# Performance work log

Measured on AMD Instinct MI355X. Metric: run time of the kernel, lower is better.

Reference implementation:

```python
import jax, jax.numpy as jnp
import numpy as np

D_MODEL = 1024
N_HEADS = 16
D_K = D_MODEL // N_HEADS
D_FF = 4096
EPS = 1e-5


def setup_inputs() -> dict:
    key = jax.random.key(0)
    ks = jax.random.split(key, 16)
    s = 0.02
    d, f = D_MODEL, D_FF
    return {
        'ebd_x': jax.random.normal(ks[0], (2, 2048, d), jnp.float32),
        'Wq': jax.random.normal(ks[1], (d, d), jnp.float32) * s,
        'bq': jnp.zeros((d,), jnp.float32),
        'Wk': jax.random.normal(ks[2], (d, d), jnp.float32) * s,
        'bk': jnp.zeros((d,), jnp.float32),
        'Wv': jax.random.normal(ks[3], (d, d), jnp.float32) * s,
        'bv': jnp.zeros((d,), jnp.float32),
        'Wo': jax.random.normal(ks[4], (d, d), jnp.float32) * s,
        'bo': jnp.zeros((d,), jnp.float32),
        'W1': jax.random.normal(ks[5], (d, f), jnp.float32) * s,
        'b1': jnp.zeros((f,), jnp.float32),
        'W2': jax.random.normal(ks[6], (f, d), jnp.float32) * s,
        'b2': jnp.zeros((d,), jnp.float32),
        'g1': jnp.ones((d,), jnp.float32),
        'beta1': jnp.zeros((d,), jnp.float32),
        'g2': jnp.ones((d,), jnp.float32),
        'beta2': jnp.zeros((d,), jnp.float32),
    }


def _layernorm(x, g, b):
    mu = jnp.mean(x, axis=-1, keepdims=True)
    var = jnp.mean(jnp.square(x - mu), axis=-1, keepdims=True)
    return (x - mu) * jax.lax.rsqrt(var + EPS) * g + b


def reference(ebd_x, Wq, bq, Wk, bk, Wv, bv, Wo, bo, W1, b1, W2, b2, g1, beta1, g2, beta2):
    b, L, d = ebd_x.shape
    h, dk = N_HEADS, D_K
    # QKV projections, split heads: (b, h, L, dk)
    q = (ebd_x @ Wq + bq).reshape(b, L, h, dk).transpose(0, 2, 1, 3)
    k = (ebd_x @ Wk + bk).reshape(b, L, h, dk).transpose(0, 2, 1, 3)
    v = (ebd_x @ Wv + bv).reshape(b, L, h, dk).transpose(0, 2, 1, 3)
    scores = jnp.einsum('bhLd,bhld->bhLl', q, k) / jnp.sqrt(jnp.float32(dk))
    attn = jax.nn.softmax(scores, axis=-1)
    attn_v = jnp.einsum('bhLl,bhld->bhLd', attn, v)
    # faithful to source: reshape (b,h,L,dk) -> (b,L,d) WITHOUT transposing back
    attn_v = attn_v.reshape(b, L, d)
    attn_v = attn_v @ Wo + bo
    # dropout is identity in eval mode
    x1 = _layernorm(attn_v + ebd_x, g1, beta1)
    ff = jax.nn.gelu(x1 @ W1 + b1, approximate=False) @ W2 + b2
    return _layernorm(ff + x1, g2, beta2)
```

## Files before the change

kernel.cpp:

```cpp
#include <hip/hip_runtime.h>
#include <hip/hip_bf16.h>
#include <math.h>

typedef __bf16 bhalf;
typedef __bf16 bhalf8 __attribute__((ext_vector_type(8)));
typedef float  floatx4 __attribute__((ext_vector_type(4)));
typedef float  floatx8 __attribute__((ext_vector_type(8)));
typedef unsigned short ushort_t;
typedef unsigned short ushort8 __attribute__((ext_vector_type(8)));

#define MFMA16(a, b, c) __builtin_amdgcn_mfma_f32_16x16x32_bf16((a), (b), (c), 0, 0, 0)

__device__ __forceinline__ void gload_lds16(const bhalf* g, bhalf* l)
{
    __builtin_amdgcn_global_load_lds((const __attribute__((address_space(1))) void*)g,
                                     (__attribute__((address_space(3))) void*)l, 16, 0, 0);
}

enum { EPI_PLAIN = 0, EPI_RES = 1, EPI_GELU = 2, EPI_QKV = 3 };

__global__ __launch_bounds__(256) void detect_dtype(const ushort_t* __restrict__ x,
                                                    int* __restrict__ flag)
{
    __shared__ int tot;
    if (threadIdx.x == 0) tot = 0;
    __syncthreads();
    int cnt = 0;
#pragma unroll
    for (int it = 0; it < 8; ++it) {
        const ushort8 u = *(const ushort8*)(x + ((size_t)(it * 256 + threadIdx.x)) * 8);
#pragma unroll
        for (int j = 0; j < 8; j += 2) {
            const int e = (u[j] >> 7) & 0xFF;
            if (e >= 0x90) ++cnt;
        }
    }
    atomicAdd(&tot, cnt);
    __syncthreads();
    if (threadIdx.x == 0) flag[0] = (tot > 64) ? 1 : 0;
}

__global__ __launch_bounds__(256) void norm_x(const void* __restrict__ s,
                                              bhalf* __restrict__ d,
                                              const int* __restrict__ flag)
{
    const int i = (blockIdx.x * 256 + threadIdx.x) * 8;
    if (*flag) {
        const floatx8 v = *(const floatx8*)((const float*)s + i);
        bhalf8 o;
#pragma unroll
        for (int j = 0; j < 8; ++j) o[j] = (bhalf)v[j];
        *(bhalf8*)(d + i) = o;
    } else {
        *(ushort8*)((ushort_t*)d + i) = *(const ushort8*)((const ushort_t*)s + i);
    }
}

struct Cvt { const void* s; bhalf* d; int n; };
struct CvtArr { Cvt t[10]; };

__global__ __launch_bounds__(256) void norm_vec(CvtArr a, const int* __restrict__ flag)
{
    const Cvt c = a.t[blockIdx.y];
    const int i = (blockIdx.x * 256 + threadIdx.x) * 8;
    if (i >= c.n) return;
    if (*flag) {
        const floatx8 v = *(const floatx8*)((const float*)c.s + i);
        bhalf8 o;
#pragma unroll
        for (int j = 0; j < 8; ++j) o[j] = (bhalf)v[j];
        *(bhalf8*)(c.d + i) = o;
    } else {
        *(ushort8*)((ushort_t*)c.d + i) = *(const ushort8*)((const ushort_t*)c.s + i);
    }
}

struct TDesc { const void* src; bhalf* dst; int R, C; };
struct TDescArr { TDesc t[6]; };

__global__ __launch_bounds__(256) void transpose_all(TDescArr a, const int* __restrict__ flag)
{
    __shared__ bhalf sm[32][33];
    const int id = blockIdx.x;
    TDesc d;
    int rem;
    if (id < 4096)      { d = a.t[id >> 10]; rem = id & 1023; }
    else if (id < 8192) { d = a.t[4];        rem = id - 4096; }
    else                { d = a.t[5];        rem = id - 8192; }
    const int txc = d.C >> 5;
    const int bx = (rem % txc) * 32;
    const int by = (rem / txc) * 32;
    const int tx = threadIdx.x & 31;
    const int ty = threadIdx.x >> 5;
    if (*flag) {
        const float* fin = (const float*)d.src;
#pragma unroll
        for (int i = 0; i < 4; ++i)
            sm[ty + i * 8][tx] = (bhalf)fin[(size_t)(by + ty + i * 8) * d.C + bx + tx];
    } else {
        const bhalf* bin = (const bhalf*)d.src;
#pragma unroll
        for (int i = 0; i < 4; ++i)
            sm[ty + i * 8][tx] = bin[(size_t)(by + ty + i * 8) * d.C + bx + tx];
    }
    __syncthreads();
#pragma unroll
    for (int i = 0; i < 4; ++i)
        d.dst[(size_t)(bx + ty + i * 8) * d.R + by + tx] = sm[tx][ty + i * 8];
}

__global__ __launch_bounds__(256) void vt_transpose(const bhalf* __restrict__ Vw,
                                                    bhalf* __restrict__ Vt)
{
    __shared__ bhalf sm[32][33];
    const int bh = blockIdx.z;
    const int b = bh >> 4, h = bh & 15;
    const int tb = blockIdx.y * 32;
    const int db = blockIdx.x * 32;
    const int tx = threadIdx.x & 31;
    const int ty = threadIdx.x >> 5;
#pragma unroll
    for (int i = 0; i < 4; ++i)
        sm[ty + i * 8][tx] = Vw[(size_t)(b * 2048 + tb + ty + i * 8) * 1024 + h * 64 + db + tx];
    __syncthreads();
#pragma unroll
    for (int i = 0; i < 4; ++i)
        Vt[(size_t)(bh * 64 + db + ty + i * 8) * 2048 + tb + tx] = sm[tx][ty + i * 8];
}

template <int EPI>
__global__ __launch_bounds__(256) void gemm128(
    const bhalf* __restrict__ A, int lda,
    const bhalf* __restrict__ BT, int ldb,
    const bhalf* __restrict__ bias,
    const bhalf* __restrict__ resid,
    bhalf* __restrict__ C, int ldc, int K, int nbx,
    bhalf* __restrict__ Ck, bhalf* __restrict__ Cv)
{
    __shared__ __align__(16) bhalf As[2][128 * 64];
    __shared__ __align__(16) bhalf Bs[2][64 * 64];

    const int tid  = threadIdx.x;
    const int lane = tid & 63;
    const int w    = tid >> 6;
    const int l15  = lane & 15;
    const int q    = lane >> 4;
    const int wm   = w * 32;

    const int nwg = gridDim.x;
    const int cpx = nwg >> 3;
    const int id  = (blockIdx.x & 7) * cpx + (blockIdx.x >> 3);
    const int n0  = (id % nbx) * 64;
    const int m0  = (id / nbx) * 128;

    const int r8 = lane >> 3;
    const int c8 = lane & 7;
    const int gc = (c8 ^ r8) << 3;

    floatx4 acc[2][4];
#pragma unroll
    for (int i = 0; i < 2; ++i)
#pragma unroll
        for (int j = 0; j < 4; ++j) acc[i][j] = (floatx4){0.f, 0.f, 0.f, 0.f};

    auto stage = [&](int buf, int k0) {
#pragma unroll
        for (int i = 0; i < 4; ++i) {
            const int rb = w * 32 + i * 8;
            gload_lds16(A + (size_t)(m0 + rb + r8) * lda + k0 + gc, &As[buf][rb * 64] + lane * 8);
        }
#pragma unroll
        for (int i = 0; i < 2; ++i) {
            const int rb = w * 16 + i * 8;
            gload_lds16(BT + (size_t)(n0 + rb + r8) * ldb + k0 + gc, &Bs[buf][rb * 64] + lane * 8);
        }
    };

    stage(0, 0);
    const int NT = K >> 6;
    for (int t = 0; t < NT; ++t) {
        const int cur = t & 1;
        __syncthreads();
        if (t + 1 < NT) stage(cur ^ 1, (t + 1) << 6);

#pragma unroll
        for (int s = 0; s < 2; ++s) {
            const int pc = (((s * 4 + q) ^ (l15 & 7)) << 3);
            bhalf8 af[2], bf[4];
#pragma unroll
            for (int mt = 0; mt < 2; ++mt)
                af[mt] = *(const bhalf8*)&As[cur][(wm + mt * 16 + l15) * 64 + pc];
#pragma unroll
            for (int nt = 0; nt < 4; ++nt)
                bf[nt] = *(const bhalf8*)&Bs[cur][(nt * 16 + l15) * 64 + pc];
#pragma unroll
            for (int mt = 0; mt < 2; ++mt)
#pragma unroll
                for (int nt = 0; nt < 4; ++nt)
                    acc[mt][nt] = MFMA16(af[mt], bf[nt], acc[mt][nt]);
        }
    }

#pragma unroll
    for (int mt = 0; mt < 2; ++mt)
#pragma unroll
        for (int nt = 0; nt < 4; ++nt) {
            const int col = n0 + nt * 16 + l15;
            const float bv = (float)bias[col];
#pragma unroll
            for (int r = 0; r < 4; ++r) {
                const int row = m0 + wm + mt * 16 + q * 4 + r;
                float v = acc[mt][nt][r] + bv;
                if constexpr (EPI == EPI_RES) {
                    v += (float)resid[(size_t)row * ldc + col];
                    C[(size_t)row * ldc + col] = (bhalf)v;
                } else if constexpr (EPI == EPI_GELU) {
                    v = 0.5f * v * (1.f + erff(v * 0.70710678118654752f));
                    C[(size_t)row * ldc + col] = (bhalf)v;
                } else if constexpr (EPI == EPI_QKV) {
                    if (col < 1024)       C [(size_t)row * 1024 + col]        = (bhalf)v;
                    else if (col < 2048)  Ck[(size_t)row * 1024 + col - 1024] = (bhalf)v;
                    else                  Cv[(size_t)row * 1024 + col - 2048] = (bhalf)v;
                } else {
                    C[(size_t)row * ldc + col] = (bhalf)v;
                }
            }
        }
}

__global__ __launch_bounds__(256) void flash_attn(
    const bhalf* __restrict__ Q, const bhalf* __restrict__ Km,
    const bhalf* __restrict__ Vt, bhalf* __restrict__ ctx)
{
    __shared__ __align__(16) bhalf Ks[2][64 * 64];
    __shared__ __align__(16) bhalf Vs[2][64 * 64];

    const int tid  = threadIdx.x;
    const int lane = tid & 63;
    const int wq   = tid >> 6;
    const int l15  = lane & 15;
    const int q    = lane >> 4;
    const int bh   = blockIdx.x & 31;
    const int l0   = (blockIdx.x >> 5) * 64;
    const int b    = bh >> 4, h = bh & 15;
    const float SC = 0.125f * 1.44269504f;

    const bhalf* qp = Q + ((size_t)(b * 2048 + l0 + wq * 16 + l15)) * 1024 + h * 64 + q * 8;
    const bhalf8 aQ0 = *(const bhalf8*)qp;
    const bhalf8 aQ1 = *(const bhalf8*)(qp + 32);

    float ps = 0.f;
    floatx4 o[4];
#pragma unroll
    for (int ot = 0; ot < 4; ++ot) o[ot] = (floatx4){0.f, 0.f, 0.f, 0.f};

    const int r8 = lane >> 3;
    const int c8 = lane & 7;
    const bhalf* kbase = Km + ((size_t)(b * 2048)) * 1024 + h * 64;
    const bhalf* vbase = Vt + ((size_t)(bh * 64)) * 2048;

    auto stage = [&](int buf, int kt) {
#pragma unroll
        for (int i = 0; i < 2; ++i) {
            const int rb = wq * 16 + i * 8;
            const int fk = (((rb >> 3) << 1) ^ r8) & 7;
            gload_lds16(kbase + (size_t)(kt + rb + r8) * 1024 + ((c8 ^ fk) << 3),
                        &Ks[buf][rb * 64] + lane * 8);
            gload_lds16(vbase + (size_t)(rb + r8) * 2048 + kt + ((c8 ^ r8) << 3),
                        &Vs[buf][rb * 64] + lane * 8);
        }
    };

    stage(0, 0);
    int cur = 0;
    for (int kt = 0; kt < 2048; kt += 64) {
        __syncthreads();
        if (kt + 64 < 2048) stage(cur ^ 1, kt + 64);

        floatx4 s[4];
#pragma unroll
        for (int nt = 0; nt < 4; ++nt) {
            const int row = (nt >> 1) * 32 + (nt & 1) * 4 + ((l15 >> 2) << 3) + (l15 & 3);
            const int f = (((row >> 3) << 1) ^ row) & 7;
            const bhalf8 k0 = *(const bhalf8*)&Ks[cur][row * 64 + ((q ^ f) << 3)];
            const bhalf8 k1 = *(const bhalf8*)&Ks[cur][row * 64 + (((4 + q) ^ f) << 3)];
            floatx4 z = (floatx4){0.f, 0.f, 0.f, 0.f};
            z = MFMA16(k0, aQ0, z);
            s[nt] = MFMA16(k1, aQ1, z);
        }

        bhalf8 pa[2];
#pragma unroll
        for (int nt = 0; nt < 4; ++nt)
#pragma unroll
            for (int r = 0; r < 4; ++r) {
                const float pv = __builtin_amdgcn_exp2f(fmaf(s[nt][r], SC, -8.f));
                ps += pv;
                pa[nt >> 1][(nt & 1) * 4 + r] = (bhalf)pv;
            }

#pragma unroll
        for (int kc = 0; kc < 2; ++kc)
#pragma unroll
            for (int ot = 0; ot < 4; ++ot) {
                const bhalf8 bV = *(const bhalf8*)&Vs[cur][(ot * 16 + l15) * 64 + (((kc * 4 + q) ^ (l15 & 7)) << 3)];
                o[ot] = MFMA16(pa[kc], bV, o[ot]);
            }
        cur ^= 1;
    }

    ps += __shfl_xor(ps, 16);
    ps += __shfl_xor(ps, 32);
    const float invq = 1.f / ps;
    float inv[4];
#pragma unroll
    for (int r = 0; r < 4; ++r)
        inv[r] = __shfl(invq, (lane & 48) | (q * 4 + r));

#pragma unroll
    for (int ot = 0; ot < 4; ++ot)
#pragma unroll
        for (int r = 0; r < 4; ++r) {
            const int l = l0 + wq * 16 + q * 4 + r;
            const int kk = ot * 16 + l15;
            const int R = h * 128 + (l >> 4);
            const int Cc = (l & 15) * 64 + kk;
            ctx[((size_t)(b * 2048 + R)) * 1024 + Cc] = (bhalf)(o[ot][r] * inv[r]);
        }
}

__global__ __launch_bounds__(256) void ln_kernel(
    const bhalf* __restrict__ X, const bhalf* __restrict__ g,
    const bhalf* __restrict__ be, void* __restrict__ out, const int* __restrict__ flag)
{
    __shared__ float red[4][2];
    const int tid = threadIdx.x;
    const int wid = tid >> 6;
    const int rid = tid >> 7;
    const int lt  = tid & 127;
    const int row = blockIdx.x * 2 + rid;
    const int col = lt * 8;
    const bhalf8 xv = *(const bhalf8*)(X + (size_t)row * 1024 + col);
    float v[8], s1 = 0.f, s2 = 0.f;
#pragma unroll
    for (int i = 0; i < 8; ++i) {
        v[i] = (float)xv[i];
        s1 += v[i];
        s2 += v[i] * v[i];
    }
#pragma unroll
    for (int off = 1; off < 64; off <<= 1) {
        s1 += __shfl_xor(s1, off);
        s2 += __shfl_xor(s2, off);
    }
    if ((tid & 63) == 0) { red[wid][0] = s1; red[wid][1] = s2; }
    __syncthreads();
    const float t1 = red[rid * 2][0] + red[rid * 2 + 1][0];
    const float t2 = red[rid * 2][1] + red[rid * 2 + 1][1];
    const float mu = t1 * (1.f / 1024.f);
    const float rs = rsqrtf(t2 * (1.f / 1024.f) - mu * mu + 1e-5f);
    const bool f32 = flag && (*flag != 0);
    if (f32) {
        floatx8 ov;
#pragma unroll
        for (int i = 0; i < 8; ++i)
            ov[i] = ((v[i] - mu) * rs) * (float)g[col + i] + (float)be[col + i];
        *(floatx8*)((float*)out + (size_t)row * 1024 + col) = ov;
    } else {
        bhalf8 ov;
#pragma unroll
        for (int i = 0; i < 8; ++i)
            ov[i] = (bhalf)(((v[i] - mu) * rs) * (float)g[col + i] + (float)be[col + i]);
        *(bhalf8*)((bhalf*)out + (size_t)row * 1024 + col) = ov;
    }
}

extern "C" void kernel_launch(void* const* d_in, const int* in_sizes, int n_in,
                              void* d_out, int out_size, void* d_ws, size_t ws_size,
                              hipStream_t stream)
{
    (void)in_sizes; (void)n_in; (void)out_size; (void)ws_size;

    char* p = (char*)d_ws;
    const size_t MB = 1024 * 1024;
    int*   flag  = (int*)p;
    bhalf* vecs  = (bhalf*)(p + 128 * 1024);
    bhalf* Qw    = (bhalf*)(p + 1 * MB);
    bhalf* Kw    = (bhalf*)(p + 9 * MB);
    bhalf* Vw    = (bhalf*)(p + 17 * MB);
    bhalf* Vt    = (bhalf*)(p + 25 * MB);
    bhalf* x_n   = (bhalf*)(p + 33 * MB);
    bhalf* WqkvT = (bhalf*)(p + 41 * MB);
    bhalf* WoT   = (bhalf*)(p + 47 * MB);
    bhalf* W1T   = (bhalf*)(p + 49 * MB);
    bhalf* W2T   = (bhalf*)(p + 57 * MB);
    bhalf* ctx   = Vw;
    bhalf* ff1   = (bhalf*)(p + 17 * MB);
    bhalf* ln1   = Qw;
    bhalf* x1    = Kw;
    bhalf* ff2   = Qw;

    bhalf* bqkv  = vecs;
    bhalf* bo_n  = vecs + 1 * 4096;
    bhalf* b1_n  = vecs + 2 * 4096;
    bhalf* b2_n  = vecs + 3 * 4096;
    bhalf* g1_n  = vecs + 4 * 4096;
    bhalf* be1_n = vecs + 5 * 4096;
    bhalf* g2_n  = vecs + 6 * 4096;
    bhalf* be2_n = vecs + 7 * 4096;

    const dim3 blk(256);

    detect_dtype<<<1, blk, 0, stream>>>((const ushort_t*)d_in[0], flag);

    norm_x<<<2048, blk, 0, stream>>>(d_in[0], x_n, flag);
    CvtArr arr;
    arr.t[0] = {d_in[2],  bqkv,        1024};
    arr.t[1] = {d_in[4],  bqkv + 1024, 1024};
    arr.t[2] = {d_in[6],  bqkv + 2048, 1024};
    arr.t[3] = {d_in[8],  bo_n,        1024};
    arr.t[4] = {d_in[10], b1_n,        4096};
    arr.t[5] = {d_in[12], b2_n,        1024};
    arr.t[6] = {d_in[13], g1_n,        1024};
    arr.t[7] = {d_in[14], be1_n,       1024};
    arr.t[8] = {d_in[15], g2_n,        1024};
    arr.t[9] = {d_in[16], be2_n,       1024};
    norm_vec<<<dim3(2, 10), blk, 0, stream>>>(arr, flag);

    TDescArr td;
    td.t[0] = {d_in[1],  WqkvT,               1024, 1024};
    td.t[1] = {d_in[3],  WqkvT + 1024 * 1024, 1024, 1024};
    td.t[2] = {d_in[5],  WqkvT + 2048 * 1024, 1024, 1024};
    td.t[3] = {d_in[7],  WoT,                 1024, 1024};
    td.t[4] = {d_in[9],  W1T,                 1024, 4096};
    td.t[5] = {d_in[11], W2T,                 4096, 1024};
    transpose_all<<<12288, blk, 0, stream>>>(td, flag);

    gemm128<EPI_QKV><<<1536, blk, 0, stream>>>(
        x_n, 1024, WqkvT, 1024, bqkv, nullptr, Qw, 1024, 1024, 48, Kw, Vw);

    vt_transpose<<<dim3(2, 64, 32), blk, 0, stream>>>(Vw, Vt);

    flash_attn<<<1024, blk, 0, stream>>>(Qw, Kw, Vt, ctx);

    gemm128<EPI_RES><<<512, blk, 0, stream>>>(
        ctx, 1024, WoT, 1024, bo_n, x_n, ln1, 1024, 1024, 16, nullptr, nullptr);
    ln_kernel<<<2048, blk, 0, stream>>>(ln1, g1_n, be1_n, x1, nullptr);

    gemm128<EPI_GELU><<<2048, blk, 0, stream>>>(
        x1, 1024, W1T, 1024, b1_n, nullptr, ff1, 4096, 1024, 64, nullptr, nullptr);
    gemm128<EPI_RES><<<512, blk, 0, stream>>>(
        ff1, 4096, W2T, 4096, b2_n, x1, ff2, 1024, 4096, 16, nullptr, nullptr);
    ln_kernel<<<2048, blk, 0, stream>>>(ff2, g2_n, be2_n, d_out, flag);
}
```

Baseline: 380.2 us.

## Rewrite GEMM with 128x128 tiles, 512 threads and triple-buffered LDS pipeline

```diff
diff --git a/kernel.cpp b/kernel.cpp
--- a/kernel.cpp
+++ b/kernel.cpp
@@ -129,7 +129,7 @@
 }
 
 template <int EPI>
-__global__ __launch_bounds__(256) void gemm128(
+__global__ __launch_bounds__(512, 2) void gemm_pp(
     const bhalf* __restrict__ A, int lda,
     const bhalf* __restrict__ BT, int ldb,
     const bhalf* __restrict__ bias,
@@ -137,75 +137,102 @@
     bhalf* __restrict__ C, int ldc, int K, int nbx,
     bhalf* __restrict__ Ck, bhalf* __restrict__ Cv)
 {
-    __shared__ __align__(16) bhalf As[2][128 * 64];
-    __shared__ __align__(16) bhalf Bs[2][64 * 64];
+    extern __shared__ __align__(16) bhalf sm[];
 
     const int tid  = threadIdx.x;
     const int lane = tid & 63;
     const int w    = tid >> 6;
     const int l15  = lane & 15;
     const int q    = lane >> 4;
-    const int wm   = w * 32;
+    const int wm   = (w >> 2) * 64;
+    const int wn   = (w & 3) * 32;
 
     const int nwg = gridDim.x;
     const int cpx = nwg >> 3;
     const int id  = (blockIdx.x & 7) * cpx + (blockIdx.x >> 3);
-    const int n0  = (id % nbx) * 64;
+    const int n0  = (id % nbx) * 128;
     const int m0  = (id / nbx) * 128;
 
-    const int r8 = lane >> 3;
-    const int c8 = lane & 7;
-    const int gc = (c8 ^ r8) << 3;
-
-    floatx4 acc[2][4];
-#pragma unroll
-    for (int i = 0; i < 2; ++i)
-#pragma unroll
-        for (int j = 0; j < 4; ++j) acc[i][j] = (floatx4){0.f, 0.f, 0.f, 0.f};
+    const int r6  = tid >> 3;
+    const int c8t = tid & 7;
+    const bhalf* gA[2]; const bhalf* gB[2]; int lA[2], lB[2];
+#pragma unroll
+    for (int i = 0; i < 2; ++i) {
+        const int row = i * 64 + r6;
+        const int gc  = (c8t ^ (r6 & 7)) << 3;
+        gA[i] = A  + (size_t)(m0 + row) * lda + gc;
+        gB[i] = BT + (size_t)(n0 + row) * ldb + gc;
+        lA[i] = row * 64 + c8t * 8;
+        lB[i] = row * 64 + c8t * 8;
+    }
+
+    floatx4 acc[4][2];
+#pragma unroll
+    for (int i = 0; i < 4; ++i)
+#pragma unroll
+        for (int j = 0; j < 2; ++j) acc[i][j] = (floatx4){0.f, 0.f, 0.f, 0.f};
 
     auto stage = [&](int buf, int k0) {
-#pragma unroll
-        for (int i = 0; i < 4; ++i) {
-            const int rb = w * 32 + i * 8;
-            gload_lds16(A + (size_t)(m0 + rb + r8) * lda + k0 + gc, &As[buf][rb * 64] + lane * 8);
-        }
-#pragma unroll
-        for (int i = 0; i < 2; ++i) {
-            const int rb = w * 16 + i * 8;
-            gload_lds16(BT + (size_t)(n0 + rb + r8) * ldb + k0 + gc, &Bs[buf][rb * 64] + lane * 8);
-        }
+        bhalf* as = sm + buf * 8192;
+        bhalf* bs = sm + 24576 + buf * 8192;
+        gload_lds16(gA[0] + k0, as + lA[0]);
+        gload_lds16(gA[1] + k0, as + lA[1]);
+        gload_lds16(gB[0] + k0, bs + lB[0]);
+        gload_lds16(gB[1] + k0, bs + lB[1]);
     };
 
     stage(0, 0);
+    stage(1, 64);
+    asm volatile("s_waitcnt vmcnt(4)" ::: "memory");
+    __builtin_amdgcn_s_barrier();
+    asm volatile("" ::: "memory");
+
     const int NT = K >> 6;
     for (int t = 0; t < NT; ++t) {
-        const int cur = t & 1;
-        __syncthreads();
-        if (t + 1 < NT) stage(cur ^ 1, (t + 1) << 6);
-
-#pragma unroll
-        for (int s = 0; s < 2; ++s) {
-            const int pc = (((s * 4 + q) ^ (l15 & 7)) << 3);
-            bhalf8 af[2], bf[4];
-#pragma unroll
-            for (int mt = 0; mt < 2; ++mt)
-                af[mt] = *(const bhalf8*)&As[cur][(wm + mt * 16 + l15) * 64 + pc];
-#pragma unroll
-            for (int nt = 0; nt < 4; ++nt)
-                bf[nt] = *(const bhalf8*)&Bs[cur][(nt * 16 + l15) * 64 + pc];
-#pragma unroll
-            for (int mt = 0; mt < 2; ++mt)
-#pragma unroll
-                for (int nt = 0; nt < 4; ++nt)
-                    acc[mt][nt] = MFMA16(af[mt], bf[nt], acc[mt][nt]);
-        }
-    }
-
-#pragma unroll
-    for (int mt = 0; mt < 2; ++mt)
-#pragma unroll
-        for (int nt = 0; nt < 4; ++nt) {
-            const int col = n0 + nt * 16 + l15;
+        const int buf = t % 3;
+        const bhalf* as = sm + buf * 8192;
+        const bhalf* bs = sm + 24576 + buf * 8192;
+
+        bhalf8 af[2][4], bf[2][2];
+#pragma unroll
+        for (int ks = 0; ks < 2; ++ks) {
+            const int pc = (((ks * 4 + q) ^ (l15 & 7)) << 3);
+#pragma unroll
+            for (int mt = 0; mt < 4; ++mt)
+                af[ks][mt] = *(const bhalf8*)&as[(wm + mt * 16 + l15) * 64 + pc];
+#pragma unroll
+            for (int nt = 0; nt < 2; ++nt)
+                bf[ks][nt] = *(const bhalf8*)&bs[(wn + nt * 16 + l15) * 64 + pc];
+        }
+
+        if (t + 2 < NT) stage((t + 2) % 3, (t + 2) << 6);
+
+        __builtin_amdgcn_s_setprio(1);
+#pragma unroll
+        for (int ks = 0; ks < 2; ++ks)
+#pragma unroll
+            for (int mt = 0; mt < 4; ++mt)
+#pragma unroll
+                for (int nt = 0; nt < 2; ++nt)
+                    acc[mt][nt] = MFMA16(af[ks][mt], bf[ks][nt], acc[mt][nt]);
+        __builtin_amdgcn_s_setprio(0);
+
+        if (t + 2 < NT) {
+            asm volatile("s_waitcnt vmcnt(4)" ::: "memory");
+        } else if (t + 1 < NT) {
+            asm volatile("s_waitcnt vmcnt(0)" ::: "memory");
+        }
+        if (t + 1 < NT) {
+            __builtin_amdgcn_s_barrier();
+            asm volatile("" ::: "memory");
+        }
+    }
+
+#pragma unroll
+    for (int mt = 0; mt < 4; ++mt)
+#pragma unroll
+        for (int nt = 0; nt < 2; ++nt) {
+            const int col = n0 + wn + nt * 16 + l15;
             const float bv = (float)bias[col];
 #pragma unroll
             for (int r = 0; r < 4; ++r) {
@@ -409,7 +436,19 @@
     bhalf* g2_n  = vecs + 6 * 4096;
     bhalf* be2_n = vecs + 7 * 4096;
 
+    static bool attr_done = false;
+    if (!attr_done) {
+        hipFuncSetAttribute((const void*)gemm_pp<EPI_QKV>,
+                            hipFuncAttributeMaxDynamicSharedMemorySize, 98304);
+        hipFuncSetAttribute((const void*)gemm_pp<EPI_GELU>,
+                            hipFuncAttributeMaxDynamicSharedMemorySize, 98304);
+        hipFuncSetAttribute((const void*)gemm_pp<EPI_RES>,
+                            hipFuncAttributeMaxDynamicSharedMemorySize, 98304);
+        attr_done = true;
+    }
+
     const dim3 blk(256);
+    const dim3 blk512(512);
 
     detect_dtype<<<1, blk, 0, stream>>>((const ushort_t*)d_in[0], flag);
 
@@ -436,20 +475,20 @@
     td.t[5] = {d_in[11], W2T,                 4096, 1024};
     transpose_all<<<12288, blk, 0, stream>>>(td, flag);
 
-    gemm128<EPI_QKV><<<1536, blk, 0, stream>>>(
-        x_n, 1024, WqkvT, 1024, bqkv, nullptr, Qw, 1024, 1024, 48, Kw, Vw);
+    gemm_pp<EPI_QKV><<<768, blk512, 98304, stream>>>(
+        x_n, 1024, WqkvT, 1024, bqkv, nullptr, Qw, 1024, 1024, 24, Kw, Vw);
 
     vt_transpose<<<dim3(2, 64, 32), blk, 0, stream>>>(Vw, Vt);
 
     flash_attn<<<1024, blk, 0, stream>>>(Qw, Kw, Vt, ctx);
 
-    gemm128<EPI_RES><<<512, blk, 0, stream>>>(
-        ctx, 1024, WoT, 1024, bo_n, x_n, ln1, 1024, 1024, 16, nullptr, nullptr);
+    gemm_pp<EPI_RES><<<256, blk512, 98304, stream>>>(
+        ctx, 1024, WoT, 1024, bo_n, x_n, ln1, 1024, 1024, 8, nullptr, nullptr);
     ln_kernel<<<2048, blk, 0, stream>>>(ln1, g1_n, be1_n, x1, nullptr);
 
-    gemm128<EPI_GELU><<<2048, blk, 0, stream>>>(
-        x1, 1024, W1T, 1024, b1_n, nullptr, ff1, 4096, 1024, 64, nullptr, nullptr);
-    gemm128<EPI_RES><<<512, blk, 0, stream>>>(
-        ff1, 4096, W2T, 4096, b2_n, x1, ff2, 1024, 4096, 16, nullptr, nullptr);
+    gemm_pp<EPI_GELU><<<1024, blk512, 98304, stream>>>(
+        x1, 1024, W1T, 1024, b1_n, nullptr, ff1, 4096, 1024, 32, nullptr, nullptr);
+    gemm_pp<EPI_RES><<<256, blk512, 98304, stream>>>(
+        ff1, 4096, W2T, 4096, b2_n, x1, ff2, 1024, 4096, 8, nullptr, nullptr);
     ln_kernel<<<2048, blk, 0, stream>>>(ff2, g2_n, be2_n, d_out, flag);
 }
```

New measurement: 360.7 us. 1.05x faster.

## Triple-buffer GEMM LDS staging with prefetch distance two and single barrier

Applied to the files above, without the earlier changes.

```diff
diff --git a/kernel.cpp b/kernel.cpp
--- a/kernel.cpp
+++ b/kernel.cpp
@@ -129,7 +129,7 @@
 }
 
 template <int EPI>
-__global__ __launch_bounds__(256) void gemm128(
+__global__ __launch_bounds__(256) void gemm_3b(
     const bhalf* __restrict__ A, int lda,
     const bhalf* __restrict__ BT, int ldb,
     const bhalf* __restrict__ bias,
@@ -137,8 +137,7 @@
     bhalf* __restrict__ C, int ldc, int K, int nbx,
     bhalf* __restrict__ Ck, bhalf* __restrict__ Cv)
 {
-    __shared__ __align__(16) bhalf As[2][128 * 64];
-    __shared__ __align__(16) bhalf Bs[2][64 * 64];
+    extern __shared__ __align__(16) bhalf sm[];
 
     const int tid  = threadIdx.x;
     const int lane = tid & 63;
@@ -163,41 +162,68 @@
 #pragma unroll
         for (int j = 0; j < 4; ++j) acc[i][j] = (floatx4){0.f, 0.f, 0.f, 0.f};
 
+    const bhalf* Ab = A  + (size_t)(m0 + r8) * lda + gc;
+    const bhalf* Bb = BT + (size_t)(n0 + r8) * ldb + gc;
+
     auto stage = [&](int buf, int k0) {
+        bhalf* as = sm + buf * 8192;
+        bhalf* bs = sm + 24576 + buf * 4096;
 #pragma unroll
         for (int i = 0; i < 4; ++i) {
             const int rb = w * 32 + i * 8;
-            gload_lds16(A + (size_t)(m0 + rb + r8) * lda + k0 + gc, &As[buf][rb * 64] + lane * 8);
+            gload_lds16(Ab + (size_t)rb * lda + k0, as + rb * 64 + lane * 8);
         }
 #pragma unroll
         for (int i = 0; i < 2; ++i) {
             const int rb = w * 16 + i * 8;
-            gload_lds16(BT + (size_t)(n0 + rb + r8) * ldb + k0 + gc, &Bs[buf][rb * 64] + lane * 8);
+            gload_lds16(Bb + (size_t)rb * ldb + k0, bs + rb * 64 + lane * 8);
         }
     };
 
     stage(0, 0);
+    stage(1, 64);
+    asm volatile("s_waitcnt vmcnt(6)" ::: "memory");
+    __builtin_amdgcn_s_barrier();
+    asm volatile("" ::: "memory");
+
     const int NT = K >> 6;
     for (int t = 0; t < NT; ++t) {
-        const int cur = t & 1;
-        __syncthreads();
-        if (t + 1 < NT) stage(cur ^ 1, (t + 1) << 6);
-
-#pragma unroll
-        for (int s = 0; s < 2; ++s) {
-            const int pc = (((s * 4 + q) ^ (l15 & 7)) << 3);
-            bhalf8 af[2], bf[4];
+        const int buf = t % 3;
+        const bhalf* as = sm + buf * 8192;
+        const bhalf* bs = sm + 24576 + buf * 4096;
+
+        bhalf8 af[2][2], bf[2][4];
+#pragma unroll
+        for (int ks = 0; ks < 2; ++ks) {
+            const int pc = (((ks * 4 + q) ^ (l15 & 7)) << 3);
 #pragma unroll
             for (int mt = 0; mt < 2; ++mt)
-                af[mt] = *(const bhalf8*)&As[cur][(wm + mt * 16 + l15) * 64 + pc];
+                af[ks][mt] = *(const bhalf8*)&as[(wm + mt * 16 + l15) * 64 + pc];
 #pragma unroll
             for (int nt = 0; nt < 4; ++nt)
-                bf[nt] = *(const bhalf8*)&Bs[cur][(nt * 16 + l15) * 64 + pc];
+                bf[ks][nt] = *(const bhalf8*)&bs[(nt * 16 + l15) * 64 + pc];
+        }
+
+        if (t + 2 < NT) stage((t + 2) % 3, (t + 2) << 6);
+
+        __builtin_amdgcn_s_setprio(1);
+#pragma unroll
+        for (int ks = 0; ks < 2; ++ks)
 #pragma unroll
             for (int mt = 0; mt < 2; ++mt)
 #pragma unroll
                 for (int nt = 0; nt < 4; ++nt)
-                    acc[mt][nt] = MFMA16(af[mt], bf[nt], acc[mt][nt]);
+                    acc[mt][nt] = MFMA16(af[ks][mt], bf[ks][nt], acc[mt][nt]);
+        __builtin_amdgcn_s_setprio(0);
+
+        if (t + 2 < NT) {
+            asm volatile("s_waitcnt vmcnt(6)" ::: "memory");
+        } else if (t + 1 < NT) {
+            asm volatile("s_waitcnt vmcnt(0)" ::: "memory");
+        }
+        if (t + 1 < NT) {
+            __builtin_amdgcn_s_barrier();
+            asm volatile("" ::: "memory");
         }
     }
 
@@ -409,6 +435,17 @@
     bhalf* g2_n  = vecs + 6 * 4096;
     bhalf* be2_n = vecs + 7 * 4096;
 
+    static bool attr_done = false;
+    if (!attr_done) {
+        hipFuncSetAttribute((const void*)gemm_3b<EPI_QKV>,
+                            hipFuncAttributeMaxDynamicSharedMemorySize, 73728);
+        hipFuncSetAttribute((const void*)gemm_3b<EPI_RES>,
+                            hipFuncAttributeMaxDynamicSharedMemorySize, 73728);
+        hipFuncSetAttribute((const void*)gemm_3b<EPI_GELU>,
+                            hipFuncAttributeMaxDynamicSharedMemorySize, 73728);
+        attr_done = true;
+    }
+
     const dim3 blk(256);
 
     detect_dtype<<<1, blk, 0, stream>>>((const ushort_t*)d_in[0], flag);
@@ -436,20 +473,20 @@
     td.t[5] = {d_in[11], W2T,                 4096, 1024};
     transpose_all<<<12288, blk, 0, stream>>>(td, flag);
 
-    gemm128<EPI_QKV><<<1536, blk, 0, stream>>>(
+    gemm_3b<EPI_QKV><<<1536, blk, 73728, stream>>>(
         x_n, 1024, WqkvT, 1024, bqkv, nullptr, Qw, 1024, 1024, 48, Kw, Vw);
 
     vt_transpose<<<dim3(2, 64, 32), blk, 0, stream>>>(Vw, Vt);
 
     flash_attn<<<1024, blk, 0, stream>>>(Qw, Kw, Vt, ctx);
 
-    gemm128<EPI_RES><<<512, blk, 0, stream>>>(
+    gemm_3b<EPI_RES><<<512, blk, 73728, stream>>>(
         ctx, 1024, WoT, 1024, bo_n, x_n, ln1, 1024, 1024, 16, nullptr, nullptr);
     ln_kernel<<<2048, blk, 0, stream>>>(ln1, g1_n, be1_n, x1, nullptr);
 
-    gemm128<EPI_GELU><<<2048, blk, 0, stream>>>(
+    gemm_3b<EPI_GELU><<<2048, blk, 73728, stream>>>(
         x1, 1024, W1T, 1024, b1_n, nullptr, ff1, 4096, 1024, 64, nullptr, nullptr);
-    gemm128<EPI_RES><<<512, blk, 0, stream>>>(
+    gemm_3b<EPI_RES><<<512, blk, 73728, stream>>>(
         ff1, 4096, W2T, 4096, b2_n, x1, ff2, 1024, 4096, 16, nullptr, nullptr);
     ln_kernel<<<2048, blk, 0, stream>>>(ff2, g2_n, be2_n, d_out, flag);
 }
```

Result: faster. 371.5 us (-2.3%).
